# Kernel optimization log

Measured on AMD Instinct MI355X. Metric: run time of the kernel, lower is better.

Reference implementation:

```python
import jax, jax.numpy as jnp
import numpy as np

N, F = 400000, 128
M = 100000
DENSE = [256, 256, 128]


def setup_inputs() -> dict:
    key = jax.random.key(0)
    ks = jax.random.split(key, 8)
    x = jax.random.normal(ks[0], (N, F), dtype=jnp.float32)
    sel_idx = jax.random.randint(ks[1], (M, 1), 0, N, dtype=jnp.int32)
    # Dense layer params, scaled like glorot-ish init
    W0 = jax.random.normal(ks[2], (F, DENSE[0]), dtype=jnp.float32) * (1.0 / np.sqrt(F))
    b0 = jnp.zeros((DENSE[0],), dtype=jnp.float32)
    W1 = jax.random.normal(ks[3], (DENSE[0], DENSE[1]), dtype=jnp.float32) * (1.0 / np.sqrt(DENSE[0]))
    b1 = jnp.zeros((DENSE[1],), dtype=jnp.float32)
    W2 = jax.random.normal(ks[4], (DENSE[1], DENSE[2]), dtype=jnp.float32) * (1.0 / np.sqrt(DENSE[1]))
    b2 = jnp.zeros((DENSE[2],), dtype=jnp.float32)
    return {"x": x, "sel_idx": sel_idx, "W0": W0, "b0": b0,
            "W1": W1, "b1": b1, "W2": W2, "b2": b2}


def reference(x, sel_idx, W0, b0, W1, b1, W2, b2):
    idx = sel_idx[:, 0]                       # [M]
    up = x[idx]                               # gather_nd -> [M, F]
    up = jax.nn.elu(up @ W0 + b0)             # [M, 256]
    up = jax.nn.elu(up @ W1 + b1)             # [M, 256]
    up = jax.nn.elu(up @ W2 + b2)             # [M, F]
    # x += scatter_nd(sel_idx, up, shape(x))
    return x + jnp.zeros_like(x).at[idx].add(up)
```

## Files before the change

kernel.cpp:

```cpp
#include <hip/hip_runtime.h>
#include <hip/hip_bf16.h>

#define NROWS 400000
#define MSEL  100000
#define FDIM  128
#define D0 256
#define D1 256
#define D2 128

typedef __attribute__((ext_vector_type(8))) short short8;
typedef __attribute__((ext_vector_type(4))) float f32x4;
typedef __attribute__((ext_vector_type(4))) unsigned short ushort4v;
typedef __attribute__((ext_vector_type(2))) unsigned int uint2v;

__device__ __forceinline__ unsigned short f2bf(float f) {
    unsigned int u = __float_as_uint(f);
    unsigned int r = (u + 0x7fffu + ((u >> 16) & 1u)) >> 16;
    return (unsigned short)r;
}

__device__ __forceinline__ unsigned int pk2bf(float a, float b) {
    __hip_bfloat162 h = __float22bfloat162_rn(make_float2(a, b));
    return *(unsigned int*)&h;
}

__device__ __forceinline__ float elu(float v) {
    return v > 0.f ? v : (__expf(v) - 1.f);
}

__global__ void pack_weights(const float* __restrict__ W0,
                             const float* __restrict__ W1,
                             const float* __restrict__ W2,
                             short* __restrict__ out) {
    int e = blockIdx.x * 256 + threadIdx.x;
    if (e >= 131072) return;
    const float* W; int N; int base; int le;
    if (e < 32768)       { W = W0; N = 256; base = 0;     le = e; }
    else if (e < 98304)  { W = W1; N = 256; base = 32768; le = e - 32768; }
    else                 { W = W2; N = 128; base = 98304; le = e - 98304; }
    int t    = le >> 9;
    int r    = le & 511;
    int lane = r >> 3;
    int j    = r & 7;
    int ntiles = N >> 4;
    int kt = t / ntiles, nt = t % ntiles;
    int k = kt * 32 + (lane >> 4) * 8 + j;
    int n = nt * 16 + (lane & 15);
    out[base + le] = (short)f2bf(W[k * N + n]);
}

__global__ void copy_x(const float4* __restrict__ x, float4* __restrict__ out, int n4) {
    int i = blockIdx.x * blockDim.x + threadIdx.x;
    int stride = gridDim.x * blockDim.x;
    for (; i < n4; i += stride) out[i] = x[i];
}

__global__ void init_head(int* __restrict__ head) {
    int i = blockIdx.x * 256 + threadIdx.x;
    int s = gridDim.x * 256;
    for (; i < NROWS; i += s) head[i] = -1;
}

__global__ void build_links(const int* __restrict__ sel,
                            int* __restrict__ head, int* __restrict__ next) {
    int j = blockIdx.x * 256 + threadIdx.x;
    if (j < MSEL) {
        int r = sel[j];
        next[j] = atomicExch(head + r, j);
    }
}

template <bool SPLIT>
__global__ __launch_bounds__(256) void mlp_compute(
    const float* __restrict__ x, const int* __restrict__ sel,
    const short* __restrict__ wp,
    const float* __restrict__ b0v, const float* __restrict__ b1v,
    const float* __restrict__ b2v,
    unsigned short* __restrict__ upOut, float* __restrict__ out) {
    __shared__ __align__(16) short lds[16384];

    const int tid  = threadIdx.x;
    const int lane = tid & 63;
    const int w    = tid >> 6;
    const int rowBase = blockIdx.x * 32;
    const int lm = lane & 15;
    const int kq = lane >> 4;
    const int sxz = (lm & 7) << 3;

    const short* W0p = wp;
    const short* W1p = wp + 32768;
    const short* W2p = wp + 98304;

    const float4* xv = (const float4*)x;
    float4 gv[4];
    int grow[4], gseg[4];
    #pragma unroll
    for (int it = 0; it < 4; it++) {
        int i = it * 256 + tid;
        grow[it] = i >> 5; gseg[it] = i & 31;
        gv[it] = xv[(size_t)sel[rowBase + grow[it]] * 32 + gseg[it]];
    }

    short8 B0[4][4];
    #pragma unroll
    for (int kt = 0; kt < 4; kt++)
        #pragma unroll
        for (int ntl = 0; ntl < 4; ntl++)
            B0[kt][ntl] = *(const short8*)(W0p + ((kt * 16 + (w * 4 + ntl)) * 512 + lane * 8));

    #pragma unroll
    for (int it = 0; it < 4; it++) {
        uint2v p = { pk2bf(gv[it].x, gv[it].y), pk2bf(gv[it].z, gv[it].w) };
        *(uint2v*)(&lds[(grow[it] * 128 + gseg[it] * 4) ^ ((grow[it] & 7) << 3)]) = p;
    }
    __syncthreads();

    const f32x4 zero4 = {0.f, 0.f, 0.f, 0.f};

    short8 B1a[8][2];
    {
        f32x4 acc[2][4];
        #pragma unroll
        for (int i = 0; i < 2; i++)
            #pragma unroll
            for (int j = 0; j < 4; j++) acc[i][j] = zero4;
        #pragma unroll
        for (int rt = 0; rt < 2; rt++) {
            short8 a[4];
            int rowA = rt * 16 + lm;
            #pragma unroll
            for (int kt = 0; kt < 4; kt++)
                a[kt] = *(const short8*)(&lds[(rowA * 128 + kt * 32 + kq * 8) ^ sxz]);
            #pragma unroll
            for (int ntl = 0; ntl < 4; ntl++)
                #pragma unroll
                for (int kt = 0; kt < 4; kt++)
                    acc[rt][ntl] = __builtin_amdgcn_mfma_f32_16x16x32_bf16(a[kt], B0[kt][ntl], acc[rt][ntl], 0, 0, 0);
        }
        #pragma unroll
        for (int kt = 0; kt < 8; kt++)
            #pragma unroll
            for (int p = 0; p < 2; p++)
                B1a[kt][p] = *(const short8*)(W1p + ((kt * 16 + (w * 4 + p)) * 512 + lane * 8));

        #pragma unroll
        for (int ntl = 0; ntl < 4; ntl++) {
            int col = (w * 4 + ntl) * 16 + lm;
            float bias = b0v[col];
            #pragma unroll
            for (int rt = 0; rt < 2; rt++) {
                float v0 = elu(acc[rt][ntl][0] + bias);
                float v1 = elu(acc[rt][ntl][1] + bias);
                float v2 = elu(acc[rt][ntl][2] + bias);
                float v3 = elu(acc[rt][ntl][3] + bias);
                unsigned int u01 = pk2bf(v0, v1), u23 = pk2bf(v2, v3);
                int row = rt * 16 + kq * 4;
                lds[4096 + (((row+0) * 256 + col) ^ (((row+0) & 7) << 3))] = (short)(u01 & 0xffff);
                lds[4096 + (((row+1) * 256 + col) ^ (((row+1) & 7) << 3))] = (short)(u01 >> 16);
                lds[4096 + (((row+2) * 256 + col) ^ (((row+2) & 7) << 3))] = (short)(u23 & 0xffff);
                lds[4096 + (((row+3) * 256 + col) ^ (((row+3) & 7) << 3))] = (short)(u23 >> 16);
            }
        }
    }
    __syncthreads();

    short8 B2[8][2];
    {
        short8 B1b[8][2];
        #pragma unroll
        for (int kt = 0; kt < 8; kt++)
            #pragma unroll
            for (int p = 0; p < 2; p++)
                B1b[kt][p] = *(const short8*)(W1p + ((kt * 16 + (w * 4 + 2 + p)) * 512 + lane * 8));

        f32x4 acc[2][2];
        #pragma unroll
        for (int i = 0; i < 2; i++)
            #pragma unroll
            for (int j = 0; j < 2; j++) acc[i][j] = zero4;
        #pragma unroll
        for (int rt = 0; rt < 2; rt++) {
            short8 a[8];
            int rowA = rt * 16 + lm;
            #pragma unroll
            for (int kt = 0; kt < 8; kt++)
                a[kt] = *(const short8*)(&lds[4096 + ((rowA * 256 + kt * 32 + kq * 8) ^ sxz)]);
            #pragma unroll
            for (int p = 0; p < 2; p++)
                #pragma unroll
                for (int kt = 0; kt < 8; kt++)
                    acc[rt][p] = __builtin_amdgcn_mfma_f32_16x16x32_bf16(a[kt], B1a[kt][p], acc[rt][p], 0, 0, 0);
        }
        #pragma unroll
        for (int p = 0; p < 2; p++) {
            int col = (w * 4 + p) * 16 + lm;
            float bias = b1v[col];
            #pragma unroll
            for (int rt = 0; rt < 2; rt++) {
                float v0 = elu(acc[rt][p][0] + bias);
                float v1 = elu(acc[rt][p][1] + bias);
                float v2 = elu(acc[rt][p][2] + bias);
                float v3 = elu(acc[rt][p][3] + bias);
                unsigned int u01 = pk2bf(v0, v1), u23 = pk2bf(v2, v3);
                int row = rt * 16 + kq * 4;
                int hb = rt ? 0 : 12288;
                lds[hb + ((((row+0) & 15) * 256 + col) ^ (((row+0) & 7) << 3))] = (short)(u01 & 0xffff);
                lds[hb + ((((row+1) & 15) * 256 + col) ^ (((row+1) & 7) << 3))] = (short)(u01 >> 16);
                lds[hb + ((((row+2) & 15) * 256 + col) ^ (((row+2) & 7) << 3))] = (short)(u23 & 0xffff);
                lds[hb + ((((row+3) & 15) * 256 + col) ^ (((row+3) & 7) << 3))] = (short)(u23 >> 16);
            }
        }

        #pragma unroll
        for (int i = 0; i < 2; i++)
            #pragma unroll
            for (int j = 0; j < 2; j++) acc[i][j] = zero4;
        #pragma unroll
        for (int rt = 0; rt < 2; rt++) {
            short8 a[8];
            int rowA = rt * 16 + lm;
            #pragma unroll
            for (int kt = 0; kt < 8; kt++)
                a[kt] = *(const short8*)(&lds[4096 + ((rowA * 256 + kt * 32 + kq * 8) ^ sxz)]);
            #pragma unroll
            for (int p = 0; p < 2; p++)
                #pragma unroll
                for (int kt = 0; kt < 8; kt++)
                    acc[rt][p] = __builtin_amdgcn_mfma_f32_16x16x32_bf16(a[kt], B1b[kt][p], acc[rt][p], 0, 0, 0);
        }
        #pragma unroll
        for (int kt = 0; kt < 8; kt++)
            #pragma unroll
            for (int ntl = 0; ntl < 2; ntl++)
                B2[kt][ntl] = *(const short8*)(W2p + ((kt * 8 + (w * 2 + ntl)) * 512 + lane * 8));

        #pragma unroll
        for (int p = 0; p < 2; p++) {
            int col = (w * 4 + 2 + p) * 16 + lm;
            float bias = b1v[col];
            #pragma unroll
            for (int rt = 0; rt < 2; rt++) {
                float v0 = elu(acc[rt][p][0] + bias);
                float v1 = elu(acc[rt][p][1] + bias);
                float v2 = elu(acc[rt][p][2] + bias);
                float v3 = elu(acc[rt][p][3] + bias);
                unsigned int u01 = pk2bf(v0, v1), u23 = pk2bf(v2, v3);
                int row = rt * 16 + kq * 4;
                int hb = rt ? 0 : 12288;
                lds[hb + ((((row+0) & 15) * 256 + col) ^ (((row+0) & 7) << 3))] = (short)(u01 & 0xffff);
                lds[hb + ((((row+1) & 15) * 256 + col) ^ (((row+1) & 7) << 3))] = (short)(u01 >> 16);
                lds[hb + ((((row+2) & 15) * 256 + col) ^ (((row+2) & 7) << 3))] = (short)(u23 & 0xffff);
                lds[hb + ((((row+3) & 15) * 256 + col) ^ (((row+3) & 7) << 3))] = (short)(u23 >> 16);
            }
        }
    }
    __syncthreads();

    {
        f32x4 acc[2][2];
        #pragma unroll
        for (int i = 0; i < 2; i++)
            #pragma unroll
            for (int j = 0; j < 2; j++) acc[i][j] = zero4;
        #pragma unroll
        for (int rt = 0; rt < 2; rt++) {
            short8 a[8];
            int rowA = rt * 16 + lm;
            int hb = rt ? 0 : 12288;
            #pragma unroll
            for (int kt = 0; kt < 8; kt++)
                a[kt] = *(const short8*)(&lds[hb + (((rowA & 15) * 256 + kt * 32 + kq * 8) ^ sxz)]);
            #pragma unroll
            for (int ntl = 0; ntl < 2; ntl++)
                #pragma unroll
                for (int kt = 0; kt < 8; kt++)
                    acc[rt][ntl] = __builtin_amdgcn_mfma_f32_16x16x32_bf16(a[kt], B2[kt][ntl], acc[rt][ntl], 0, 0, 0);
        }
        #pragma unroll
        for (int ntl = 0; ntl < 2; ntl++) {
            int col = (w * 2 + ntl) * 16 + lm;
            float bias = b2v[col];
            #pragma unroll
            for (int rt = 0; rt < 2; rt++)
                #pragma unroll
                for (int r = 0; r < 4; r++) {
                    int row = rt * 16 + kq * 4 + r;
                    float v = elu(acc[rt][ntl][r] + bias);
                    if (SPLIT) {
                        lds[4096 + row * 128 + col] = (short)f2bf(v);
                    } else {
                        atomicAdd(out + (size_t)sel[rowBase + row] * 128 + col, v);
                    }
                }
        }
    }
    if (SPLIT) {
        __syncthreads();
        const short8* s8 = (const short8*)(&lds[4096]);
        short8* u8 = (short8*)(upOut + (size_t)rowBase * 128);
        u8[tid]       = s8[tid];
        u8[tid + 256] = s8[tid + 256];
    }
}

__global__ __launch_bounds__(256) void merge_out(
    const float2* __restrict__ x2, const unsigned int* __restrict__ up32,
    const int* __restrict__ head, const int* __restrict__ next,
    float2* __restrict__ out2) {
    int wid  = blockIdx.x * 4 + (threadIdx.x >> 6);
    int lane = threadIdx.x & 63;
    int wstride = gridDim.x * 4;
    for (int row = wid; row < NROWS; row += wstride) {
        float2 v = x2[(size_t)row * 64 + lane];
        int j = head[row];
        while (j >= 0) {
            unsigned int u = up32[(size_t)j * 64 + lane];
            v.x += __uint_as_float(u << 16);
            v.y += __uint_as_float(u & 0xffff0000u);
            j = next[j];
        }
        out2[(size_t)row * 64 + lane] = v;
    }
}

extern "C" void kernel_launch(void* const* d_in, const int* in_sizes, int n_in,
                              void* d_out, int out_size, void* d_ws, size_t ws_size,
                              hipStream_t stream) {
    const float* x   = (const float*)d_in[0];
    const int*   sel = (const int*)d_in[1];
    const float* W0  = (const float*)d_in[2];
    const float* b0  = (const float*)d_in[3];
    const float* W1  = (const float*)d_in[4];
    const float* b1  = (const float*)d_in[5];
    const float* W2  = (const float*)d_in[6];
    const float* b2  = (const float*)d_in[7];
    float* out = (float*)d_out;

    char* wsb = (char*)d_ws;
    short* wp          = (short*)wsb;
    unsigned short* up = (unsigned short*)(wsb + 262144);
    int* head          = (int*)(wsb + 262144 + (size_t)MSEL * 256);
    int* nxt           = head + NROWS;
    const size_t need  = 262144 + (size_t)MSEL * 256 + (size_t)NROWS * 4 + (size_t)MSEL * 4;

    pack_weights<<<512, 256, 0, stream>>>(W0, W1, W2, wp);
    if (ws_size >= need) {
        init_head<<<1024, 256, 0, stream>>>(head);
        build_links<<<(MSEL + 255) / 256, 256, 0, stream>>>(sel, head, nxt);
        mlp_compute<true><<<MSEL / 32, 256, 0, stream>>>(x, sel, wp, b0, b1, b2, up, out);
        merge_out<<<4096, 256, 0, stream>>>((const float2*)x, (const unsigned int*)up,
                                            head, nxt, (float2*)out);
    } else {
        copy_x<<<4096, 256, 0, stream>>>((const float4*)x, (float4*)out, NROWS * FDIM / 4);
        mlp_compute<false><<<MSEL / 32, 256, 0, stream>>>(x, sel, wp, b0, b1, b2, up, out);
    }
}
```

Before: 151.3 us.

## Merge prep kernels and pre-gather x into MFMA-fragment bf16 layout

Fuses weight packing with head initialization, and link building with a new gather pass into two prep kernels, which cuts the launch count. The new gather pass pre-converts the selected x rows to bf16 in the MFMA A-operand fragment layout. The MLP kernel then loads layer-0 A fragments straight from global memory, skipping the indexed gather, the LDS staging and one barrier. LDS regions are remapped to match. The cost is an extra 25.6MB workspace buffer that is written and then read back, plus a much larger workspace requirement.

```diff
diff --git a/kernel.cpp b/kernel.cpp
--- a/kernel.cpp
+++ b/kernel.cpp
@@ -10,7 +10,6 @@
 
 typedef __attribute__((ext_vector_type(8))) short short8;
 typedef __attribute__((ext_vector_type(4))) float f32x4;
-typedef __attribute__((ext_vector_type(4))) unsigned short ushort4v;
 typedef __attribute__((ext_vector_type(2))) unsigned int uint2v;
 
 __device__ __forceinline__ unsigned short f2bf(float f) {
@@ -28,25 +27,50 @@
     return v > 0.f ? v : (__expf(v) - 1.f);
 }
 
-__global__ void pack_weights(const float* __restrict__ W0,
-                             const float* __restrict__ W1,
-                             const float* __restrict__ W2,
-                             short* __restrict__ out) {
-    int e = blockIdx.x * 256 + threadIdx.x;
-    if (e >= 131072) return;
-    const float* W; int N; int base; int le;
-    if (e < 32768)       { W = W0; N = 256; base = 0;     le = e; }
-    else if (e < 98304)  { W = W1; N = 256; base = 32768; le = e - 32768; }
-    else                 { W = W2; N = 128; base = 98304; le = e - 98304; }
-    int t    = le >> 9;
-    int r    = le & 511;
-    int lane = r >> 3;
-    int j    = r & 7;
-    int ntiles = N >> 4;
-    int kt = t / ntiles, nt = t % ntiles;
-    int k = kt * 32 + (lane >> 4) * 8 + j;
-    int n = nt * 16 + (lane & 15);
-    out[base + le] = (short)f2bf(W[k * N + n]);
+__global__ void prep1(const float* __restrict__ W0,
+                      const float* __restrict__ W1,
+                      const float* __restrict__ W2,
+                      short* __restrict__ wp, int* __restrict__ head) {
+    int bid = blockIdx.x;
+    if (bid < 512) {
+        int e = bid * 256 + threadIdx.x;
+        const float* W; int N; int base; int le;
+        if (e < 32768)       { W = W0; N = 256; base = 0;     le = e; }
+        else if (e < 98304)  { W = W1; N = 256; base = 32768; le = e - 32768; }
+        else                 { W = W2; N = 128; base = 98304; le = e - 98304; }
+        int t    = le >> 9;
+        int r    = le & 511;
+        int lane = r >> 3;
+        int j    = r & 7;
+        int ntiles = N >> 4;
+        int kt = t / ntiles, nt = t % ntiles;
+        int k = kt * 32 + (lane >> 4) * 8 + j;
+        int n = nt * 16 + (lane & 15);
+        wp[base + le] = (short)f2bf(W[k * N + n]);
+    } else {
+        int i = (bid - 512) * 256 + threadIdx.x;
+        if (i < NROWS) head[i] = -1;
+    }
+}
+
+__global__ void prep2(const int* __restrict__ sel, const float* __restrict__ x,
+                      int* __restrict__ head, int* __restrict__ next,
+                      unsigned int* __restrict__ xf32) {
+    int bid = blockIdx.x;
+    if (bid < 391) {
+        int j = bid * 256 + threadIdx.x;
+        if (j < MSEL) next[j] = atomicExch(head + sel[j], j);
+    } else {
+        int g = (bid - 391) * 256 + threadIdx.x;
+        int j = g >> 5, seg = g & 31;
+        float4 v = ((const float4*)x)[(size_t)sel[j] * 32 + seg];
+        int k0 = seg * 4;
+        int lane = (j & 15) + ((k0 >> 3) & 3) * 16;
+        int e = k0 & 7;
+        int idx = ((((j >> 4) * 4 + (k0 >> 5)) * 512 + lane * 8 + e) >> 1);
+        xf32[idx]     = pk2bf(v.x, v.y);
+        xf32[idx + 1] = pk2bf(v.z, v.w);
+    }
 }
 
 __global__ void copy_x(const float4* __restrict__ x, float4* __restrict__ out, int n4) {
@@ -55,23 +79,9 @@
     for (; i < n4; i += stride) out[i] = x[i];
 }
 
-__global__ void init_head(int* __restrict__ head) {
-    int i = blockIdx.x * 256 + threadIdx.x;
-    int s = gridDim.x * 256;
-    for (; i < NROWS; i += s) head[i] = -1;
-}
-
-__global__ void build_links(const int* __restrict__ sel,
-                            int* __restrict__ head, int* __restrict__ next) {
-    int j = blockIdx.x * 256 + threadIdx.x;
-    if (j < MSEL) {
-        int r = sel[j];
-        next[j] = atomicExch(head + r, j);
-    }
-}
-
 template <bool SPLIT>
 __global__ __launch_bounds__(256) void mlp_compute(
+    const short* __restrict__ xf,
     const float* __restrict__ x, const int* __restrict__ sel,
     const short* __restrict__ wp,
     const float* __restrict__ b0v, const float* __restrict__ b1v,
@@ -91,14 +101,13 @@
     const short* W1p = wp + 32768;
     const short* W2p = wp + 98304;
 
-    const float4* xv = (const float4*)x;
-    float4 gv[4];
-    int grow[4], gseg[4];
-    #pragma unroll
-    for (int it = 0; it < 4; it++) {
-        int i = it * 256 + tid;
-        grow[it] = i >> 5; gseg[it] = i & 31;
-        gv[it] = xv[(size_t)sel[rowBase + grow[it]] * 32 + gseg[it]];
+    short8 A0[2][4];
+    if constexpr (SPLIT) {
+        #pragma unroll
+        for (int rt = 0; rt < 2; rt++)
+            #pragma unroll
+            for (int kt = 0; kt < 4; kt++)
+                A0[rt][kt] = *(const short8*)(xf + (((size_t)blockIdx.x * 2 + rt) * 4 + kt) * 512 + lane * 8);
     }
 
     short8 B0[4][4];
@@ -108,12 +117,18 @@
         for (int ntl = 0; ntl < 4; ntl++)
             B0[kt][ntl] = *(const short8*)(W0p + ((kt * 16 + (w * 4 + ntl)) * 512 + lane * 8));
 
-    #pragma unroll
-    for (int it = 0; it < 4; it++) {
-        uint2v p = { pk2bf(gv[it].x, gv[it].y), pk2bf(gv[it].z, gv[it].w) };
-        *(uint2v*)(&lds[(grow[it] * 128 + gseg[it] * 4) ^ ((grow[it] & 7) << 3)]) = p;
-    }
-    __syncthreads();
+    if constexpr (!SPLIT) {
+        const float4* xv = (const float4*)x;
+        #pragma unroll
+        for (int it = 0; it < 4; it++) {
+            int i = it * 256 + tid;
+            int row = i >> 5, seg = i & 31;
+            float4 v = xv[(size_t)sel[rowBase + row] * 32 + seg];
+            uint2v p = { pk2bf(v.x, v.y), pk2bf(v.z, v.w) };
+            *(uint2v*)(&lds[8192 + ((row * 128 + seg * 4) ^ ((row & 7) << 3))]) = p;
+        }
+        __syncthreads();
+    }
 
     const f32x4 zero4 = {0.f, 0.f, 0.f, 0.f};
 
@@ -127,10 +142,14 @@
         #pragma unroll
         for (int rt = 0; rt < 2; rt++) {
             short8 a[4];
-            int rowA = rt * 16 + lm;
-            #pragma unroll
-            for (int kt = 0; kt < 4; kt++)
-                a[kt] = *(const short8*)(&lds[(rowA * 128 + kt * 32 + kq * 8) ^ sxz]);
+            #pragma unroll
+            for (int kt = 0; kt < 4; kt++) {
+                if constexpr (SPLIT) a[kt] = A0[rt][kt];
+                else {
+                    int rowA = rt * 16 + lm;
+                    a[kt] = *(const short8*)(&lds[8192 + ((rowA * 128 + kt * 32 + kq * 8) ^ sxz)]);
+                }
+            }
             #pragma unroll
             for (int ntl = 0; ntl < 4; ntl++)
                 #pragma unroll
@@ -155,10 +174,10 @@
                 float v3 = elu(acc[rt][ntl][3] + bias);
                 unsigned int u01 = pk2bf(v0, v1), u23 = pk2bf(v2, v3);
                 int row = rt * 16 + kq * 4;
-                lds[4096 + (((row+0) * 256 + col) ^ (((row+0) & 7) << 3))] = (short)(u01 & 0xffff);
-                lds[4096 + (((row+1) * 256 + col) ^ (((row+1) & 7) << 3))] = (short)(u01 >> 16);
-                lds[4096 + (((row+2) * 256 + col) ^ (((row+2) & 7) << 3))] = (short)(u23 & 0xffff);
-                lds[4096 + (((row+3) * 256 + col) ^ (((row+3) & 7) << 3))] = (short)(u23 >> 16);
+                lds[(((row+0) * 256 + col) ^ (((row+0) & 7) << 3))] = (short)(u01 & 0xffff);
+                lds[(((row+1) * 256 + col) ^ (((row+1) & 7) << 3))] = (short)(u01 >> 16);
+                lds[(((row+2) * 256 + col) ^ (((row+2) & 7) << 3))] = (short)(u23 & 0xffff);
+                lds[(((row+3) * 256 + col) ^ (((row+3) & 7) << 3))] = (short)(u23 >> 16);
             }
         }
     }
@@ -184,7 +203,7 @@
             int rowA = rt * 16 + lm;
             #pragma unroll
             for (int kt = 0; kt < 8; kt++)
-                a[kt] = *(const short8*)(&lds[4096 + ((rowA * 256 + kt * 32 + kq * 8) ^ sxz)]);
+                a[kt] = *(const short8*)(&lds[(rowA * 256 + kt * 32 + kq * 8) ^ sxz]);
             #pragma unroll
             for (int p = 0; p < 2; p++)
                 #pragma unroll
@@ -203,11 +222,10 @@
                 float v3 = elu(acc[rt][p][3] + bias);
                 unsigned int u01 = pk2bf(v0, v1), u23 = pk2bf(v2, v3);
                 int row = rt * 16 + kq * 4;
-                int hb = rt ? 0 : 12288;
-                lds[hb + ((((row+0) & 15) * 256 + col) ^ (((row+0) & 7) << 3))] = (short)(u01 & 0xffff);
-                lds[hb + ((((row+1) & 15) * 256 + col) ^ (((row+1) & 7) << 3))] = (short)(u01 >> 16);
-                lds[hb + ((((row+2) & 15) * 256 + col) ^ (((row+2) & 7) << 3))] = (short)(u23 & 0xffff);
-                lds[hb + ((((row+3) & 15) * 256 + col) ^ (((row+3) & 7) << 3))] = (short)(u23 >> 16);
+                lds[8192 + (((row+0) * 256 + col) ^ (((row+0) & 7) << 3))] = (short)(u01 & 0xffff);
+                lds[8192 + (((row+1) * 256 + col) ^ (((row+1) & 7) << 3))] = (short)(u01 >> 16);
+                lds[8192 + (((row+2) * 256 + col) ^ (((row+2) & 7) << 3))] = (short)(u23 & 0xffff);
+                lds[8192 + (((row+3) * 256 + col) ^ (((row+3) & 7) << 3))] = (short)(u23 >> 16);
             }
         }
 
@@ -221,7 +239,7 @@
             int rowA = rt * 16 + lm;
             #pragma unroll
             for (int kt = 0; kt < 8; kt++)
-                a[kt] = *(const short8*)(&lds[4096 + ((rowA * 256 + kt * 32 + kq * 8) ^ sxz)]);
+                a[kt] = *(const short8*)(&lds[(rowA * 256 + kt * 32 + kq * 8) ^ sxz]);
             #pragma unroll
             for (int p = 0; p < 2; p++)
                 #pragma unroll
@@ -246,11 +264,10 @@
                 float v3 = elu(acc[rt][p][3] + bias);
                 unsigned int u01 = pk2bf(v0, v1), u23 = pk2bf(v2, v3);
                 int row = rt * 16 + kq * 4;
-                int hb = rt ? 0 : 12288;
-                lds[hb + ((((row+0) & 15) * 256 + col) ^ (((row+0) & 7) << 3))] = (short)(u01 & 0xffff);
-                lds[hb + ((((row+1) & 15) * 256 + col) ^ (((row+1) & 7) << 3))] = (short)(u01 >> 16);
-                lds[hb + ((((row+2) & 15) * 256 + col) ^ (((row+2) & 7) << 3))] = (short)(u23 & 0xffff);
-                lds[hb + ((((row+3) & 15) * 256 + col) ^ (((row+3) & 7) << 3))] = (short)(u23 >> 16);
+                lds[8192 + (((row+0) * 256 + col) ^ (((row+0) & 7) << 3))] = (short)(u01 & 0xffff);
+                lds[8192 + (((row+1) * 256 + col) ^ (((row+1) & 7) << 3))] = (short)(u01 >> 16);
+                lds[8192 + (((row+2) * 256 + col) ^ (((row+2) & 7) << 3))] = (short)(u23 & 0xffff);
+                lds[8192 + (((row+3) * 256 + col) ^ (((row+3) & 7) << 3))] = (short)(u23 >> 16);
             }
         }
     }
@@ -266,10 +283,9 @@
         for (int rt = 0; rt < 2; rt++) {
             short8 a[8];
             int rowA = rt * 16 + lm;
-            int hb = rt ? 0 : 12288;
             #pragma unroll
             for (int kt = 0; kt < 8; kt++)
-                a[kt] = *(const short8*)(&lds[hb + (((rowA & 15) * 256 + kt * 32 + kq * 8) ^ sxz)]);
+                a[kt] = *(const short8*)(&lds[8192 + ((rowA * 256 + kt * 32 + kq * 8) ^ sxz)]);
             #pragma unroll
             for (int ntl = 0; ntl < 2; ntl++)
                 #pragma unroll
@@ -287,7 +303,7 @@
                     int row = rt * 16 + kq * 4 + r;
                     float v = elu(acc[rt][ntl][r] + bias);
                     if (SPLIT) {
-                        lds[4096 + row * 128 + col] = (short)f2bf(v);
+                        lds[row * 128 + col] = (short)f2bf(v);
                     } else {
                         atomicAdd(out + (size_t)sel[rowBase + row] * 128 + col, v);
                     }
@@ -296,7 +312,7 @@
     }
     if (SPLIT) {
         __syncthreads();
-        const short8* s8 = (const short8*)(&lds[4096]);
+        const short8* s8 = (const short8*)(&lds[0]);
         short8* u8 = (short8*)(upOut + (size_t)rowBase * 128);
         u8[tid]       = s8[tid];
         u8[tid + 256] = s8[tid + 256];
@@ -338,20 +354,20 @@
 
     char* wsb = (char*)d_ws;
     short* wp          = (short*)wsb;
-    unsigned short* up = (unsigned short*)(wsb + 262144);
-    int* head          = (int*)(wsb + 262144 + (size_t)MSEL * 256);
+    short* xf          = (short*)(wsb + 262144);
+    unsigned short* up = (unsigned short*)(wsb + 262144 + 25600000);
+    int* head          = (int*)(wsb + 262144 + 51200000);
     int* nxt           = head + NROWS;
-    const size_t need  = 262144 + (size_t)MSEL * 256 + (size_t)NROWS * 4 + (size_t)MSEL * 4;
-
-    pack_weights<<<512, 256, 0, stream>>>(W0, W1, W2, wp);
+    const size_t need  = 262144 + 51200000 + (size_t)NROWS * 4 + (size_t)MSEL * 4;
+
+    prep1<<<2075, 256, 0, stream>>>(W0, W1, W2, wp, head);
     if (ws_size >= need) {
-        init_head<<<1024, 256, 0, stream>>>(head);
-        build_links<<<(MSEL + 255) / 256, 256, 0, stream>>>(sel, head, nxt);
-        mlp_compute<true><<<MSEL / 32, 256, 0, stream>>>(x, sel, wp, b0, b1, b2, up, out);
+        prep2<<<12891, 256, 0, stream>>>(sel, x, head, nxt, (unsigned int*)xf);
+        mlp_compute<true><<<MSEL / 32, 256, 0, stream>>>(xf, x, sel, wp, b0, b1, b2, up, out);
         merge_out<<<4096, 256, 0, stream>>>((const float2*)x, (const unsigned int*)up,
                                             head, nxt, (float2*)out);
     } else {
         copy_x<<<4096, 256, 0, stream>>>((const float4*)x, (float4*)out, NROWS * FDIM / 4);
-        mlp_compute<false><<<MSEL / 32, 256, 0, stream>>>(x, sel, wp, b0, b1, b2, up, out);
-    }
-}
+        mlp_compute<false><<<MSEL / 32, 256, 0, stream>>>(xf, x, sel, wp, b0, b1, b2, up, out);
+    }
+}
```

Measured after the change: 152.0 us. Within noise of the previous version (+0.5%).
